# Kernel tuning notes

Measured on AMD Instinct MI355X. Metric: run time of the kernel, lower is better.

The kernel has to match this reference:

```python
import jax, jax.numpy as jnp
import numpy as np

Q_P = 127.0
EPS_LN = 1e-5
EPS_CLAMP = 1e-5


def setup_inputs() -> dict:
    key = jax.random.key(0)
    k1, k2 = jax.random.split(key)
    B, T, C_in, C_out, K = 8, 4096, 1024, 1024, 3
    x = jax.random.normal(k1, (B, T, C_in), dtype=jnp.float32)
    ln_gamma = jnp.ones((C_in,), dtype=jnp.float32)
    ln_beta = jnp.zeros((C_in,), dtype=jnp.float32)
    W = jax.random.normal(k2, (C_out, C_in, K), dtype=jnp.float32) * 0.02
    return {"x": x, "ln_gamma": ln_gamma, "ln_beta": ln_beta, "W": W}


def _layer_norm(x, g, b):
    mu = jnp.mean(x, axis=-1, keepdims=True)
    var = jnp.mean(jnp.square(x - mu), axis=-1, keepdims=True)
    return (x - mu) * jax.lax.rsqrt(var + EPS_LN) * g + b


def _activation_quant(x):
    # per-(batch,channel) abs-max over time axis (last axis of [B,C,T])
    gamma = jnp.maximum(jnp.max(jnp.abs(x), axis=-1, keepdims=True), EPS_CLAMP)
    scale = Q_P / gamma
    x_scaled = x * scale
    x_rounded = jnp.clip(jnp.round(x_scaled), -Q_P, Q_P)
    x_quant = jax.lax.stop_gradient(x_rounded - x_scaled) + x_scaled
    return x_quant, scale


def _weight_quant(w):
    beta = jnp.maximum(jnp.mean(jnp.abs(w)), EPS_CLAMP)
    w_scaled = w / beta
    w_rounded = jnp.round(jnp.clip(w_scaled, -1.0, 1.0))
    w_quant = jax.lax.stop_gradient(w_rounded - w_scaled) + w_scaled
    return w_quant, beta


def reference(x, ln_gamma, ln_beta, W):
    # x: [B, T, C_in]
    x_norm = _layer_norm(x, ln_gamma, ln_beta)
    x_t = jnp.transpose(x_norm, (0, 2, 1))  # [B, C_in, T]
    x_q, scale_x = _activation_quant(x_t)   # scale_x: [B, C_in, 1]
    w_q, beta_w = _weight_quant(W)
    y_raw = jax.lax.conv_general_dilated(
        x_q, w_q,
        window_strides=(1,), padding=[(1, 1)],
        dimension_numbers=("NCH", "OIH", "NCH"))  # [B, C_out, T]
    y = y_raw * (beta_w / scale_x)  # broadcast [B,C_in,1] over [B,C_out,T] (C_in==C_out)
    return jnp.transpose(y, (0, 2, 1))  # [B, T, C_out]
```

## Files before the change

kernel.cpp:

```cpp
#include <hip/hip_runtime.h>

#define B_  8
#define T_  4096
#define C_  1024
#define TP  4098
#define NW  (1024 * 1024)
#define NT  48

typedef __bf16 bf16x8 __attribute__((ext_vector_type(8)));
typedef float  f32x4  __attribute__((ext_vector_type(4)));

__device__ __forceinline__ unsigned short f2bf_rne(float f) {
    unsigned u = __float_as_uint(f);
    u += 0x7FFFu + ((u >> 16) & 1u);
    return (unsigned short)(u >> 16);
}

#define GLOAD16(g, l)                                                        \
    __builtin_amdgcn_global_load_lds(                                        \
        (const __attribute__((address_space(1))) void*)(g),                  \
        (__attribute__((address_space(3))) void*)(l), 16, 0, 0)

__global__ __launch_bounds__(256) void init_kernel(
    float* __restrict__ gamma_x, double* __restrict__ wsum,
    unsigned short* __restrict__ xq) {
    const int i = blockIdx.x * 256 + threadIdx.x;
    if (i < 8192) gamma_x[i] = 0.0f;
    if (i == 0) *wsum = 0.0;
    const int r16 = i >> 10;
    const int b = r16 >> 1, side = r16 & 1;
    xq[((size_t)b * TP + (size_t)side * (TP - 1)) * C_ + (i & 1023)] = 0;
}

__global__ __launch_bounds__(256) void stats_absmax_kernel(
    const float* __restrict__ x, const float* __restrict__ lng,
    const float* __restrict__ lnb, float2* __restrict__ stats,
    float* __restrict__ gamma_x) {
    const int tid = threadIdx.x;
    const int w = tid >> 6, l = tid & 63;
    const int row0 = blockIdx.x * 32;
    const int b = row0 >> 12;
    __shared__ unsigned lmax[1024];
#pragma unroll
    for (int k = 0; k < 4; ++k) lmax[tid + k * 256] = 0u;
    __syncthreads();

    const int c0 = l * 16;
    float gv[16], bv[16], m[16];
#pragma unroll
    for (int j = 0; j < 4; ++j) {
        *(float4*)&gv[j * 4] = *(const float4*)(lng + c0 + j * 4);
        *(float4*)&bv[j * 4] = *(const float4*)(lnb + c0 + j * 4);
    }
#pragma unroll
    for (int j = 0; j < 16; ++j) m[j] = 0.0f;

#pragma unroll 2
    for (int rr = 0; rr < 8; ++rr) {
        const int row = row0 + w * 8 + rr;
        const float* xr = x + (size_t)row * C_ + c0;
        float v[16];
#pragma unroll
        for (int j = 0; j < 4; ++j) *(float4*)&v[j * 4] = *(const float4*)(xr + j * 4);
        float s = 0.0f, s2 = 0.0f;
#pragma unroll
        for (int j = 0; j < 16; ++j) { s += v[j]; s2 += v[j] * v[j]; }
#pragma unroll
        for (int off = 1; off < 64; off <<= 1) {
            s  += __shfl_xor(s,  off, 64);
            s2 += __shfl_xor(s2, off, 64);
        }
        const float mu   = s * (1.0f / C_);
        const float var  = fmaxf(s2 * (1.0f / C_) - mu * mu, 0.0f);
        const float rstd = 1.0f / sqrtf(var + 1e-5f);
        if (l == 0) stats[row] = make_float2(mu, rstd);
#pragma unroll
        for (int j = 0; j < 16; ++j)
            m[j] = fmaxf(m[j], fabsf((v[j] - mu) * rstd * gv[j] + bv[j]));
    }
#pragma unroll
    for (int j = 0; j < 16; ++j) atomicMax(&lmax[c0 + j], __float_as_uint(m[j]));
    __syncthreads();
#pragma unroll
    for (int k = 0; k < 4; ++k) {
        const int c = tid + k * 256;
        atomicMax((unsigned*)(gamma_x + b * C_ + c), lmax[c]);
    }
}

__global__ __launch_bounds__(256) void wsum_kernel(
    const float* __restrict__ W, double* __restrict__ wsum) {
    size_t i = ((size_t)blockIdx.x * 256 + threadIdx.x) * 8;
    float4 a  = *(const float4*)(W + i);
    float4 b4 = *(const float4*)(W + i + 4);
    float s = fabsf(a.x) + fabsf(a.y) + fabsf(a.z) + fabsf(a.w)
            + fabsf(b4.x) + fabsf(b4.y) + fabsf(b4.z) + fabsf(b4.w);
#pragma unroll
    for (int off = 32; off > 0; off >>= 1) s += __shfl_down(s, off, 64);
    __shared__ float ps[4];
    const int wave = threadIdx.x >> 6, lane = threadIdx.x & 63;
    if (lane == 0) ps[wave] = s;
    __syncthreads();
    if (threadIdx.x == 0) atomicAdd(wsum, (double)((ps[0] + ps[1]) + (ps[2] + ps[3])));
}

__global__ __launch_bounds__(256) void wquant_kernel(
    const float* __restrict__ W, const double* __restrict__ wsum,
    unsigned short* __restrict__ wq, float* __restrict__ beta_out) {
    const int gid = blockIdx.x * 256 + threadIdx.x;
    const float beta = fmaxf((float)(*wsum * (1.0 / 3145728.0)), 1e-5f);
    if (gid == 0) *beta_out = beta;
    const float* wp = W + (size_t)gid * 3;
#pragma unroll
    for (int k = 0; k < 3; ++k) {
        float s  = wp[k] / beta;
        float r  = rintf(fminf(fmaxf(s, -1.0f), 1.0f));
        wq[(size_t)k * NW + gid] = f2bf_rne(r);
    }
}

__device__ __forceinline__ unsigned short quant1(float xv, float2 s, float g,
                                                 float be, float gam) {
    float xn = (xv - s.x) * s.y * g + be;
    float sc = 127.0f / fmaxf(gam, 1e-5f);
    float r  = rintf(xn * sc);
    r = fminf(fmaxf(r, -127.0f), 127.0f);
    return f2bf_rne(r);
}

__global__ __launch_bounds__(256) void xquant_kernel(
    const float* __restrict__ x, const float2* __restrict__ stats,
    const float* __restrict__ lng, const float* __restrict__ lnb,
    const float* __restrict__ gamma_x, unsigned short* __restrict__ xq) {
    const int row = blockIdx.x;
    const int b = row >> 12, t = row & 4095;
    const float2 s = stats[row];
    const int c = threadIdx.x * 4;
    float4 xv = *(const float4*)(x + (size_t)row * C_ + c);
    float4 gv = *(const float4*)(lng + c);
    float4 bv = *(const float4*)(lnb + c);
    float4 gm = *(const float4*)(gamma_x + b * C_ + c);
    ushort4 qv;
    qv.x = quant1(xv.x, s, gv.x, bv.x, gm.x);
    qv.y = quant1(xv.y, s, gv.y, bv.y, gm.y);
    qv.z = quant1(xv.z, s, gv.z, bv.z, gm.z);
    qv.w = quant1(xv.w, s, gv.w, bv.w, gm.w);
    *(ushort4*)(xq + ((size_t)b * TP + t + 1) * C_ + c) = qv;
}

__global__ __launch_bounds__(512, 2) void gemm_kernel(
    const unsigned short* __restrict__ xq,
    const unsigned short* __restrict__ wq,
    const float* __restrict__ gamma_x,
    const float* __restrict__ beta_p,
    float* __restrict__ out) {
    __shared__ __align__(16) unsigned short sA[2][2][8192];
    __shared__ __align__(16) unsigned short sB[2][2][8192];

    const int tid = threadIdx.x;
    const int w   = tid >> 6;
    const int l   = tid & 63;
    const int q   = l >> 4;
    const int lr  = l & 15;
    const int g8    = (q ^ ((lr >> 1) & 3)) * 8;
    const int srcg8 = ((l & 3) ^ ((l >> 3) & 3)) * 8;

    const int d  = blockIdx.x;
    const int gg = (d & 7) + ((d >> 5) << 3);
    const int nt = (d >> 3) & 3;
    const int b  = gg >> 4;
    const int t0 = (gg & 15) << 8;
    const int n0 = nt << 8;

    const int wm = (w >> 2) * 128;
    const int wn = (w & 3) * 64;

    const unsigned short* A0 = xq + (size_t)(b * TP + t0) * C_;
    const unsigned short* Bq = wq + (size_t)n0 * C_;

    f32x4 acc[8][4] = {};

#define STG(DST, GP) do {                                                         \
        GLOAD16((GP) + (size_t)(w * 16 + (l >> 2)) * C_ + srcg8, (DST) + w * 512);\
        GLOAD16((GP) + (size_t)(w * 16 + (l >> 2) + 128) * C_ + srcg8,            \
                (DST) + 4096 + w * 512);                                          \
    } while (0)
#define STG_A(S, KH) STG(&sA[(S) & 1][KH][0], A0 + (S) * 64 + (KH) * 32)
#define STG_B(S, KH) STG(&sB[(S) & 1][KH][0],                                     \
        Bq + (size_t)((S) >> 4) * NW + ((S) & 15) * 64 + (KH) * 32)

#define VM8 asm volatile("s_waitcnt vmcnt(8)" ::: "memory")
#define VM4 asm volatile("s_waitcnt vmcnt(4)" ::: "memory")
#define VM0 asm volatile("s_waitcnt vmcnt(0)" ::: "memory")
#define VMX do {} while (0)

#define PHASE(BU, MSET, KH, LOADB, VM, ...) do {                                  \
        bf16x8 af[4];                                                             \
        _Pragma("unroll")                                                         \
        for (int i2 = 0; i2 < 4; ++i2)                                            \
            af[i2] = *(const bf16x8*)&sA[BU][KH]                                  \
                [(wm + (MSET) * 64 + i2 * 16 + lr) * 32 + g8];                    \
        if (LOADB) {                                                              \
            _Pragma("unroll")                                                     \
            for (int ni = 0; ni < 4; ++ni)                                        \
                bfr[ni] = *(const bf16x8*)&sB[BU][KH]                             \
                    [(wn + ni * 16 + lr) * 32 + g8];                              \
        }                                                                         \
        __VA_ARGS__;                                                              \
        __builtin_amdgcn_s_barrier();                                             \
        asm volatile("s_waitcnt lgkmcnt(0)" ::: "memory");                        \
        __builtin_amdgcn_sched_barrier(0);                                        \
        __builtin_amdgcn_s_setprio(1);                                            \
        _Pragma("unroll")                                                         \
        for (int mi = 0; mi < 4; ++mi)                                            \
            _Pragma("unroll")                                                     \
            for (int ni = 0; ni < 4; ++ni)                                        \
                acc[(MSET) * 4 + mi][ni] = __builtin_amdgcn_mfma_f32_16x16x32_bf16(\
                    af[mi], bfr[ni], acc[(MSET) * 4 + mi][ni], 0, 0, 0);          \
        __builtin_amdgcn_s_setprio(0);                                            \
        VM;                                                                       \
        __builtin_amdgcn_s_barrier();                                             \
    } while (0)

#define TILE_STEP(KT, BU, DO1, DO2, VM1, VM3) do {                                \
        PHASE(BU, 0, 0, 1, VMX, { if (DO1) { STG_A((KT) + 1, 1); } });            \
        PHASE(BU, 1, 0, 0, VM1, { if (DO1) { STG_B((KT) + 1, 1); } });            \
        PHASE(BU, 0, 1, 1, VMX, { if (DO2) { STG_A((KT) + 2, 0); } });            \
        PHASE(BU, 1, 1, 0, VM3, { if (DO2) { STG_B((KT) + 2, 0); } });            \
    } while (0)

    STG_A(0, 0); STG_B(0, 0);
    STG_A(0, 1); STG_B(0, 1);
    STG_A(1, 0); STG_B(1, 0);
    VM8;
    __builtin_amdgcn_s_barrier();

    bf16x8 bfr[4];
#pragma unroll 1
    for (int kt = 0; kt < 46; kt += 2) {
        TILE_STEP(kt,     0, true, true, VM8, VM8);
        TILE_STEP(kt + 1, 1, true, true, VM8, VM8);
    }
    TILE_STEP(46, 0, true,  false, VM8, VM4);
    TILE_STEP(47, 1, false, false, VM0, VMX);

    const float beta = *beta_p;
#pragma unroll
    for (int ni = 0; ni < 4; ++ni) {
        const int o = n0 + wn + ni * 16 + lr;
        const float sc = beta * fmaxf(gamma_x[b * C_ + o], 1e-5f) * (1.0f / 127.0f);
#pragma unroll
        for (int mi = 0; mi < 8; ++mi) {
#pragma unroll
            for (int r = 0; r < 4; ++r) {
                const int t = t0 + wm + mi * 16 + q * 4 + r;
                out[(size_t)(b * T_ + t) * C_ + o] = acc[mi][ni][r] * sc;
            }
        }
    }
#undef STG
#undef STG_A
#undef STG_B
#undef PHASE
#undef TILE_STEP
}

extern "C" void kernel_launch(void* const* d_in, const int* in_sizes, int n_in,
                              void* d_out, int out_size, void* d_ws, size_t ws_size,
                              hipStream_t stream) {
    const float* x   = (const float*)d_in[0];
    const float* lng = (const float*)d_in[1];
    const float* lnb = (const float*)d_in[2];
    const float* W   = (const float*)d_in[3];
    float* out = (float*)d_out;

    char* ws = (char*)d_ws;
    float2*         stats  = (float2*)(ws + 0);
    float*          gamma  = (float*) (ws + 262144);
    double*         wsum   = (double*)(ws + 294912);
    float*          beta   = (float*) (ws + 294920);
    unsigned short* wq     = (unsigned short*)(ws + 294928);
    unsigned short* xq     = (unsigned short*)(ws + 6586384);

    init_kernel        <<<64,    256, 0, stream>>>(gamma, wsum, xq);
    stats_absmax_kernel<<<1024,  256, 0, stream>>>(x, lng, lnb, stats, gamma);
    wsum_kernel        <<<1536,  256, 0, stream>>>(W, wsum);
    wquant_kernel      <<<4096,  256, 0, stream>>>(W, wsum, wq, beta);
    xquant_kernel      <<<32768, 256, 0, stream>>>(x, stats, lng, lnb, gamma, xq);
    gemm_kernel        <<<dim3(512), 512, 0, stream>>>(xq, wq, gamma, beta, out);
}
```

Before: 509.9 us.

## Software-pipeline LDS fragment reads into MFMA loop and replace global atomicMax reduction

The GEMM main loop is restructured so the A fragments for the next phase are read from LDS between MFMA rows, and B fragments are prefetched after each phase. This drops one barrier per phase and overlaps LDS latency with matrix math, at the cost of extra live registers and changed vmcnt thresholds. Separately, the per-batch abs-max no longer uses global float atomicMax. Each block now writes partial maxima into the output buffer used as scratch, and a small extra kernel reduces them. That removes the gamma zero-init but adds one launch.

```diff
diff --git a/kernel.cpp b/kernel.cpp
--- a/kernel.cpp
+++ b/kernel.cpp
@@ -22,10 +22,8 @@
         (__attribute__((address_space(3))) void*)(l), 16, 0, 0)
 
 __global__ __launch_bounds__(256) void init_kernel(
-    float* __restrict__ gamma_x, double* __restrict__ wsum,
-    unsigned short* __restrict__ xq) {
+    double* __restrict__ wsum, unsigned short* __restrict__ xq) {
     const int i = blockIdx.x * 256 + threadIdx.x;
-    if (i < 8192) gamma_x[i] = 0.0f;
     if (i == 0) *wsum = 0.0;
     const int r16 = i >> 10;
     const int b = r16 >> 1, side = r16 & 1;
@@ -35,11 +33,10 @@
 __global__ __launch_bounds__(256) void stats_absmax_kernel(
     const float* __restrict__ x, const float* __restrict__ lng,
     const float* __restrict__ lnb, float2* __restrict__ stats,
-    float* __restrict__ gamma_x) {
+    float* __restrict__ gpart) {
     const int tid = threadIdx.x;
     const int w = tid >> 6, l = tid & 63;
     const int row0 = blockIdx.x * 32;
-    const int b = row0 >> 12;
     __shared__ unsigned lmax[1024];
 #pragma unroll
     for (int k = 0; k < 4; ++k) lmax[tid + k * 256] = 0u;
@@ -84,8 +81,19 @@
 #pragma unroll
     for (int k = 0; k < 4; ++k) {
         const int c = tid + k * 256;
-        atomicMax((unsigned*)(gamma_x + b * C_ + c), lmax[c]);
-    }
+        gpart[(size_t)blockIdx.x * 1024 + c] = __uint_as_float(lmax[c]);
+    }
+}
+
+__global__ __launch_bounds__(256) void gamma_reduce_kernel(
+    const float* __restrict__ gpart, float* __restrict__ gamma_x) {
+    const int c = (blockIdx.x & 3) * 256 + threadIdx.x;
+    const int b = blockIdx.x >> 2;
+    const float* p = gpart + (size_t)b * 128 * 1024 + c;
+    float m = 0.0f;
+#pragma unroll 8
+    for (int i = 0; i < 128; ++i) m = fmaxf(m, p[(size_t)i * 1024]);
+    gamma_x[b * 1024 + c] = m;
 }
 
 __global__ __launch_bounds__(256) void wsum_kernel(
@@ -179,6 +187,15 @@
     const unsigned short* Bq = wq + (size_t)n0 * C_;
 
     f32x4 acc[8][4] = {};
+    bf16x8 af[4], bf[4];
+
+#define RD_A(MI, ABU, AKH, AMS)                                                   \
+    af[MI] = *(const bf16x8*)&sA[ABU][AKH][(wm + (AMS) * 64 + (MI) * 16 + lr) * 32 + g8]
+#define RD_B_ALL(BBU, BKH) do {                                                   \
+        _Pragma("unroll")                                                         \
+        for (int ni = 0; ni < 4; ++ni)                                            \
+            bf[ni] = *(const bf16x8*)&sB[BBU][BKH][(wn + ni * 16 + lr) * 32 + g8];\
+    } while (0)
 
 #define STG(DST, GP) do {                                                         \
         GLOAD16((GP) + (size_t)(w * 16 + (l >> 2)) * C_ + srcg8, (DST) + w * 512);\
@@ -190,59 +207,59 @@
         Bq + (size_t)((S) >> 4) * NW + ((S) & 15) * 64 + (KH) * 32)
 
 #define VM8 asm volatile("s_waitcnt vmcnt(8)" ::: "memory")
+#define VM6 asm volatile("s_waitcnt vmcnt(6)" ::: "memory")
 #define VM4 asm volatile("s_waitcnt vmcnt(4)" ::: "memory")
 #define VM0 asm volatile("s_waitcnt vmcnt(0)" ::: "memory")
 #define VMX do {} while (0)
 
-#define PHASE(BU, MSET, KH, LOADB, VM, ...) do {                                  \
-        bf16x8 af[4];                                                             \
-        _Pragma("unroll")                                                         \
-        for (int i2 = 0; i2 < 4; ++i2)                                            \
-            af[i2] = *(const bf16x8*)&sA[BU][KH]                                  \
-                [(wm + (MSET) * 64 + i2 * 16 + lr) * 32 + g8];                    \
-        if (LOADB) {                                                              \
-            _Pragma("unroll")                                                     \
-            for (int ni = 0; ni < 4; ++ni)                                        \
-                bfr[ni] = *(const bf16x8*)&sB[BU][KH]                             \
-                    [(wn + ni * 16 + lr) * 32 + g8];                              \
-        }                                                                         \
-        __VA_ARGS__;                                                              \
-        __builtin_amdgcn_s_barrier();                                             \
+#define PH(AM, DOAF, ABU, AMS, AKH, DOBF, BBU, BKH, STGC, VMC, BAR) do {          \
+        STGC;                                                                     \
         asm volatile("s_waitcnt lgkmcnt(0)" ::: "memory");                        \
         __builtin_amdgcn_sched_barrier(0);                                        \
         __builtin_amdgcn_s_setprio(1);                                            \
         _Pragma("unroll")                                                         \
-        for (int mi = 0; mi < 4; ++mi)                                            \
+        for (int mi = 0; mi < 4; ++mi) {                                          \
             _Pragma("unroll")                                                     \
             for (int ni = 0; ni < 4; ++ni)                                        \
-                acc[(MSET) * 4 + mi][ni] = __builtin_amdgcn_mfma_f32_16x16x32_bf16(\
-                    af[mi], bfr[ni], acc[(MSET) * 4 + mi][ni], 0, 0, 0);          \
+                acc[(AM) * 4 + mi][ni] = __builtin_amdgcn_mfma_f32_16x16x32_bf16( \
+                    af[mi], bf[ni], acc[(AM) * 4 + mi][ni], 0, 0, 0);             \
+            if (DOAF) { RD_A(mi, ABU, AKH, AMS); }                                \
+            __builtin_amdgcn_sched_barrier(0);                                    \
+        }                                                                         \
         __builtin_amdgcn_s_setprio(0);                                            \
-        VM;                                                                       \
-        __builtin_amdgcn_s_barrier();                                             \
+        if (DOBF) { RD_B_ALL(BBU, BKH); }                                         \
+        VMC;                                                                      \
+        if (BAR) { __builtin_amdgcn_s_barrier();                                  \
+                   __builtin_amdgcn_sched_barrier(0); }                           \
     } while (0)
 
-#define TILE_STEP(KT, BU, DO1, DO2, VM1, VM3) do {                                \
-        PHASE(BU, 0, 0, 1, VMX, { if (DO1) { STG_A((KT) + 1, 1); } });            \
-        PHASE(BU, 1, 0, 0, VM1, { if (DO1) { STG_B((KT) + 1, 1); } });            \
-        PHASE(BU, 0, 1, 1, VMX, { if (DO2) { STG_A((KT) + 2, 0); } });            \
-        PHASE(BU, 1, 1, 0, VM3, { if (DO2) { STG_B((KT) + 2, 0); } });            \
+#define TILE(BU, S0C, S1C, S2C, S3C, VA, VB, AF3, BF3, BAR3) do {                 \
+        PH(0, 1, BU, 1, 0, 0, 0, 0, S0C, VA, 1);                                  \
+        PH(1, 1, BU, 0, 1, 1, BU, 1, S1C, VMX, 1);                                \
+        PH(0, 1, BU, 1, 1, 0, 0, 0, S2C, VB, 1);                                  \
+        PH(1, AF3, (BU) ^ 1, 0, 0, BF3, (BU) ^ 1, 0, S3C, VMX, BAR3);             \
     } while (0)
+
+#define TILE_ST(KT, BU)                                                           \
+    TILE(BU, { STG_A((KT) + 1, 1); }, { STG_B((KT) + 1, 1); },                    \
+             { STG_A((KT) + 2, 0); }, { STG_B((KT) + 2, 0); }, VM6, VM6, 1, 1, 1)
 
     STG_A(0, 0); STG_B(0, 0);
     STG_A(0, 1); STG_B(0, 1);
     STG_A(1, 0); STG_B(1, 0);
     VM8;
     __builtin_amdgcn_s_barrier();
-
-    bf16x8 bfr[4];
+    __builtin_amdgcn_sched_barrier(0);
+    RD_A(0, 0, 0, 0); RD_A(1, 0, 0, 0); RD_A(2, 0, 0, 0); RD_A(3, 0, 0, 0);
+    RD_B_ALL(0, 0);
+
 #pragma unroll 1
     for (int kt = 0; kt < 46; kt += 2) {
-        TILE_STEP(kt,     0, true, true, VM8, VM8);
-        TILE_STEP(kt + 1, 1, true, true, VM8, VM8);
-    }
-    TILE_STEP(46, 0, true,  false, VM8, VM4);
-    TILE_STEP(47, 1, false, false, VM0, VMX);
+        TILE_ST(kt, 0);
+        TILE_ST(kt + 1, 1);
+    }
+    TILE(0, { STG_A(47, 1); }, { STG_B(47, 1); }, {}, {}, VM6, VM4, 1, 1, 1);
+    TILE(1, {}, {}, {}, {}, VM0, VMX, 0, 0, 0);
 
     const float beta = *beta_p;
 #pragma unroll
@@ -258,11 +275,14 @@
             }
         }
     }
+#undef RD_A
+#undef RD_B_ALL
 #undef STG
 #undef STG_A
 #undef STG_B
-#undef PHASE
-#undef TILE_STEP
+#undef PH
+#undef TILE
+#undef TILE_ST
 }
 
 extern "C" void kernel_launch(void* const* d_in, const int* in_sizes, int n_in,
@@ -281,9 +301,11 @@
     float*          beta   = (float*) (ws + 294920);
     unsigned short* wq     = (unsigned short*)(ws + 294928);
     unsigned short* xq     = (unsigned short*)(ws + 6586384);
-
-    init_kernel        <<<64,    256, 0, stream>>>(gamma, wsum, xq);
-    stats_absmax_kernel<<<1024,  256, 0, stream>>>(x, lng, lnb, stats, gamma);
+    float*          gpart  = out;
+
+    init_kernel        <<<64,    256, 0, stream>>>(wsum, xq);
+    stats_absmax_kernel<<<1024,  256, 0, stream>>>(x, lng, lnb, stats, gpart);
+    gamma_reduce_kernel<<<32,    256, 0, stream>>>(gpart, gamma);
     wsum_kernel        <<<1536,  256, 0, stream>>>(W, wsum);
     wquant_kernel      <<<4096,  256, 0, stream>>>(W, wsum, wq, beta);
     xquant_kernel      <<<32768, 256, 0, stream>>>(x, stats, lng, lnb, gamma, xq);
```

New measurement: 524.0 us. 2.8% more time.
